# Kernel optimization log

Hardware: AMD Instinct MI355X
Metric: run time of the kernel (lower is better)

## Reference

```python
import jax, jax.numpy as jnp
import numpy as np

LAMBDA = 1.0          # lambda_param
SIGMA = 1.0           # RBF bandwidth (sigkernel convention: exp(-||x-y||^2 / sigma))
DYADIC_ORDER = 2
F = 2 ** DYADIC_ORDER # dyadic refinement factor per time axis

B, M_POP, DIM, SEQ_LEN = 4, 16, 8, 65


def _rbf_gram(X, Y):
    # X: (m, L, d), Y: (n, L, d) -> static kernel Gram (m, n, L, L)
    sx = jnp.sum(X * X, -1)                       # (m, L)
    sy = jnp.sum(Y * Y, -1)                       # (n, L)
    inner = jnp.einsum('isd,jtd->ijst', X, Y)     # (m, n, L, L)
    d2 = sx[:, None, :, None] + sy[None, :, None, :] - 2.0 * inner
    return jnp.exp(-d2 / SIGMA)


def _increments(G):
    # double increment of the static Gram over time, then dyadic refinement
    inc = G[..., 1:, 1:] + G[..., :-1, :-1] - G[..., 1:, :-1] - G[..., :-1, 1:]
    inc = jnp.repeat(jnp.repeat(inc, F, axis=-2), F, axis=-1) / (F * F)
    return inc  # (..., S, S) with S = F*(L-1)


def _solve_pde(M):
    # Goursat PDE explicit finite-difference scheme (as in sigkernel):
    # K[i+1,j+1] = (K[i+1,j]+K[i,j+1])*(1 + m/2 + m^2/12) - K[i,j]*(1 - m^2/12)
    dtype = M.dtype
    S = M.shape[0]

    def row_step(prev_row, m_row):
        def cell(k_left, inp):
            k00, k01, m = inp
            a = 1.0 + 0.5 * m + m * m * (1.0 / 12.0)
            b = 1.0 - m * m * (1.0 / 12.0)
            k_new = (k_left + k01) * a - k00 * b
            return k_new, k_new
        _, tail = jax.lax.scan(cell, jnp.asarray(1.0, dtype),
                               (prev_row[:-1], prev_row[1:], m_row))
        new_row = jnp.concatenate([jnp.ones((1,), dtype), tail])
        return new_row, None

    row0 = jnp.ones((S + 1,), dtype)
    last_row, _ = jax.lax.scan(row_step, row0, M)
    return last_row[-1]


def _gram_sig(X, Y):
    # signature kernel Gram matrix: X (m,L,d), Y (n,L,d) -> (m,n)
    Minc = _increments(_rbf_gram(X, Y))
    return jax.vmap(jax.vmap(_solve_pde))(Minc)


def setup_inputs() -> dict:
    key = jax.random.key(0)
    k1, k2 = jax.random.split(key)
    generated_samples = jax.random.normal(k1, (B, M_POP, DIM, SEQ_LEN), dtype=jnp.float32)
    real_sample = jax.random.normal(k2, (B, DIM, SEQ_LEN), dtype=jnp.float32)
    return {"generated_samples": generated_samples, "real_sample": real_sample}


def reference(generated_samples, real_sample):
    # generated_samples: (B, m, dim, L); real_sample: (B, dim, L)
    gen = jnp.swapaxes(generated_samples, -1, -2)          # (B, m, L, d)
    real = jnp.swapaxes(real_sample, -1, -2)[:, None]      # (B, 1, L, d)
    m = gen.shape[1]
    K_XX = jax.vmap(_gram_sig)(gen, gen)                   # (B, m, m)
    K_XY = jax.vmap(_gram_sig)(gen, real)                  # (B, m, 1)
    self_sim = (jnp.sum(K_XX, axis=(-1, -2))
                - jnp.trace(K_XX, axis1=-2, axis2=-1)) / (m * (m - 1))
    cross_sim = jnp.mean(K_XY, axis=(-1, -2))
    return jnp.mean(LAMBDA / 2.0 * self_sim - cross_sim)
```

## Files before the change

### kernel.cpp

```cpp
#include <hip/hip_runtime.h>


#define SEQ   65
#define DIMS  8
#define MPOP  16
#define NBATCH 4
#define NPAIR_XX 120
#define NBLOCKS (NBATCH*(NPAIR_XX + MPOP))
#define MST 67

__device__ __forceinline__ float wave_shr1(float x) {
    int xi = __builtin_bit_cast(int, x);
    int r  = __builtin_amdgcn_update_dpp(xi, xi, 0x138 , 0xF, 0xF, false);
    return __builtin_bit_cast(float, r);
}

__device__ __forceinline__ int clamp63(int v) {
    return v < 0 ? 0 : (v > 63 ? 63 : v);
}

__global__ __launch_bounds__(256) void sigker_kernel(
    const float* __restrict__ gen,
    const float* __restrict__ realp,
    float* __restrict__ out)
{
    __shared__ float YsL[SEQ][DIMS];
    __shared__ float MmL[64 * MST];

    const int tid = threadIdx.x;
    const int I   = tid & 63;
    const int c   = tid >> 6;
    const int bid = blockIdx.x;

    int b, ii, jj; bool cross;
    if (bid < NBATCH * NPAIR_XX) {
        b = bid / NPAIR_XX;
        int p = bid % NPAIR_XX;
        int i = 0, acc = 0;
        while (p >= acc + (MPOP - 1 - i)) { acc += (MPOP - 1 - i); ++i; }
        ii = i; jj = i + 1 + (p - acc); cross = false;
    } else {
        int t = bid - NBATCH * NPAIR_XX;
        b = t / MPOP; ii = t % MPOP; jj = 0; cross = true;
    }

    const float* Xg = gen + (size_t)(b * MPOP + ii) * (DIMS * SEQ);
    const float* Yg = cross ? (realp + (size_t)b * (DIMS * SEQ))
                            : (gen + (size_t)(b * MPOP + jj) * (DIMS * SEQ));

    for (int f = tid; f < SEQ * DIMS; f += 256) {
        int d = f / SEQ, s = f - d * SEQ;
        YsL[s][d] = Yg[f];
    }
    float x0[DIMS], x1[DIMS];
    #pragma unroll
    for (int d = 0; d < DIMS; ++d) {
        x0[d] = Xg[d * SEQ + I];
        x1[d] = Xg[d * SEQ + I + 1];
    }
    __syncthreads();

    {
        float* mrow = &MmL[I * MST];
        const int t0 = c * 16;
        float e0p, e1p;
        {
            float d0 = 0.f, d1 = 0.f;
            #pragma unroll
            for (int d = 0; d < DIMS; ++d) {
                float y = YsL[t0][d];
                float a0 = x0[d] - y; d0 += a0 * a0;
                float a1 = x1[d] - y; d1 += a1 * a1;
            }
            e0p = __expf(-d0); e1p = __expf(-d1);
        }
        #pragma unroll
        for (int t = 1; t <= 16; ++t) {
            float d0 = 0.f, d1 = 0.f;
            #pragma unroll
            for (int d = 0; d < DIMS; ++d) {
                float y = YsL[t0 + t][d];
                float a0 = x0[d] - y; d0 += a0 * a0;
                float a1 = x1[d] - y; d1 += a1 * a1;
            }
            float e0 = __expf(-d0), e1 = __expf(-d1);
            mrow[t0 + t - 1] = (e1 + e0p - e1p - e0) * (1.0f / 16.0f);
            e0p = e0; e1p = e1;
        }
    }
    __syncthreads();
    if (tid >= 64) return;

    const float* mrow = &MmL[I * MST];
    float l0 = 1.f, l1 = 1.f, l2 = 1.f, l3 = 1.f;
    float b0 = 1.f, b1 = 1.f, b2 = 1.f, b3 = 1.f;
    float cnext = 1.f;

#define STEP(DTv, MV) do {                                              \
        float t0_ = wave_shr1(b0);                                      \
        float t1_ = wave_shr1(b1);                                      \
        float t2_ = wave_shr1(b2);                                      \
        float t3_ = wave_shr1(b3);                                      \
        float cc_ = cnext; cnext = t3_;                                 \
        if (I == 0) { t0_ = t1_ = t2_ = t3_ = 1.f; cc_ = 1.f; }         \
        int J_ = (DTv) - I;                                             \
        if ((unsigned)J_ < 64u) {                                       \
            if (J_ == 0) cc_ = 1.f;                                     \
            float m_   = (MV);                                          \
            float q12_ = m_ * m_ * (1.0f / 12.0f);                      \
            float a_   = 1.0f + 0.5f * m_ + q12_;                       \
            float nb_  = q12_ - 1.0f;                                   \
            float u0_ = a_ * t0_ + nb_ * cc_;                           \
            float u1_ = a_ * t1_ + nb_ * t0_;                           \
            float u2_ = a_ * t2_ + nb_ * t1_;                           \
            float u3_ = a_ * t3_ + nb_ * t2_;                           \
            float q1_ = a_ * l0 + u0_;                                  \
            float q2_ = a_ * q1_ + u1_;                                 \
            float q3_ = a_ * q2_ + u2_;                                 \
            float q4_ = a_ * q3_ + u3_;                                 \
            u0_ = a_ * q1_ + nb_ * l0;  u1_ = a_ * q2_ + nb_ * q1_;     \
            u2_ = a_ * q3_ + nb_ * q2_; u3_ = a_ * q4_ + nb_ * q3_;     \
            float r1_ = a_ * l1 + u0_;                                  \
            float r2_ = a_ * r1_ + u1_;                                 \
            float r3_ = a_ * r2_ + u2_;                                 \
            float r4_ = a_ * r3_ + u3_;                                 \
            u0_ = a_ * r1_ + nb_ * l1;  u1_ = a_ * r2_ + nb_ * r1_;     \
            u2_ = a_ * r3_ + nb_ * r2_; u3_ = a_ * r4_ + nb_ * r3_;     \
            float s1_ = a_ * l2 + u0_;                                  \
            float s2_ = a_ * s1_ + u1_;                                 \
            float s3_ = a_ * s2_ + u2_;                                 \
            float s4_ = a_ * s3_ + u3_;                                 \
            u0_ = a_ * s1_ + nb_ * l2;  u1_ = a_ * s2_ + nb_ * s1_;     \
            u2_ = a_ * s3_ + nb_ * s2_; u3_ = a_ * s4_ + nb_ * s3_;     \
            float v1_ = a_ * l3 + u0_;                                  \
            float v2_ = a_ * v1_ + u1_;                                 \
            float v3_ = a_ * v2_ + u2_;                                 \
            float v4_ = a_ * v3_ + u3_;                                 \
            b0 = v1_; b1 = v2_; b2 = v3_; b3 = v4_;                     \
            l0 = q4_; l1 = r4_; l2 = s4_; l3 = v4_;                     \
        }                                                               \
    } while (0)

    float m0 = mrow[clamp63(0 - I)];
    float m1 = mrow[clamp63(1 - I)];
    float m2 = mrow[clamp63(2 - I)];
    float m3 = mrow[clamp63(3 - I)];

    for (int g = 0; g < 32; ++g) {
        const int DT0 = g * 4;
        float n0 = mrow[clamp63(DT0 + 4 - I)];
        float n1 = mrow[clamp63(DT0 + 5 - I)];
        float n2 = mrow[clamp63(DT0 + 6 - I)];
        float n3 = mrow[clamp63(DT0 + 7 - I)];
        STEP(DT0 + 0, m0);
        STEP(DT0 + 1, m1);
        STEP(DT0 + 2, m2);
        STEP(DT0 + 3, m3);
        m0 = n0; m1 = n1; m2 = n2; m3 = n3;
    }
#undef STEP

    if (tid == 63) {
        float w = cross ? (-1.0f / 32.0f) : (1.0f / 480.0f);
        atomicAdd(out, w * b3);
    }
}

extern "C" void kernel_launch(void* const* d_in, const int* in_sizes, int n_in,
                              void* d_out, int out_size, void* d_ws, size_t ws_size,
                              hipStream_t stream) {
    const float* gen   = (const float*)d_in[0];
    const float* realp = (const float*)d_in[1];
    if (n_in >= 2 && in_sizes[0] == NBATCH * DIMS * SEQ) {
        gen   = (const float*)d_in[1];
        realp = (const float*)d_in[0];
    }
    float* out = (float*)d_out;
    hipMemsetAsync(out, 0, sizeof(float), stream);
    sigker_kernel<<<NBLOCKS, 256, 0, stream>>>(gen, realp, out);
}
```

Before: 96.28 us.

## Use single-wave blocks and replace atomic accumulation with a workspace reduction

Each block shrinks from 256 threads to one 64-lane wave. That wave computes the whole increment row per lane, which removes the block barrier and the idle waves during the PDE sweep. The atomicAdd and the memset are replaced by per-block writes to a workspace, summed by a second small reduction kernel. In exchange, each block does four times more serial Gram work per lane and the launch gains an extra kernel.

```diff
diff --git a/kernel.cpp b/kernel.cpp
--- a/kernel.cpp
+++ b/kernel.cpp
@@ -19,17 +19,16 @@
     return v < 0 ? 0 : (v > 63 ? 63 : v);
 }
 
-__global__ __launch_bounds__(256) void sigker_kernel(
+__global__ __launch_bounds__(64, 1) void sigker_kernel(
     const float* __restrict__ gen,
     const float* __restrict__ realp,
-    float* __restrict__ out)
+    float* __restrict__ ws)
 {
     __shared__ float YsL[SEQ][DIMS];
     __shared__ float MmL[64 * MST];
 
     const int tid = threadIdx.x;
-    const int I   = tid & 63;
-    const int c   = tid >> 6;
+    const int I   = tid;
     const int bid = blockIdx.x;
 
     int b, ii, jj; bool cross;
@@ -48,7 +47,7 @@
     const float* Yg = cross ? (realp + (size_t)b * (DIMS * SEQ))
                             : (gen + (size_t)(b * MPOP + jj) * (DIMS * SEQ));
 
-    for (int f = tid; f < SEQ * DIMS; f += 256) {
+    for (int f = tid; f < SEQ * DIMS; f += 64) {
         int d = f / SEQ, s = f - d * SEQ;
         YsL[s][d] = Yg[f];
     }
@@ -60,38 +59,32 @@
     }
     __syncthreads();
 
+    float* mrow = &MmL[I * MST];
+    float e0p, e1p;
     {
-        float* mrow = &MmL[I * MST];
-        const int t0 = c * 16;
-        float e0p, e1p;
-        {
-            float d0 = 0.f, d1 = 0.f;
-            #pragma unroll
-            for (int d = 0; d < DIMS; ++d) {
-                float y = YsL[t0][d];
-                float a0 = x0[d] - y; d0 += a0 * a0;
-                float a1 = x1[d] - y; d1 += a1 * a1;
-            }
-            e0p = __expf(-d0); e1p = __expf(-d1);
+        float d0 = 0.f, d1 = 0.f;
+        #pragma unroll
+        for (int d = 0; d < DIMS; ++d) {
+            float y = YsL[0][d];
+            float a0 = x0[d] - y; d0 += a0 * a0;
+            float a1 = x1[d] - y; d1 += a1 * a1;
         }
+        e0p = __expf(-d0); e1p = __expf(-d1);
+    }
+    #pragma unroll 8
+    for (int t = 1; t < SEQ; ++t) {
+        float d0 = 0.f, d1 = 0.f;
         #pragma unroll
-        for (int t = 1; t <= 16; ++t) {
-            float d0 = 0.f, d1 = 0.f;
-            #pragma unroll
-            for (int d = 0; d < DIMS; ++d) {
-                float y = YsL[t0 + t][d];
-                float a0 = x0[d] - y; d0 += a0 * a0;
-                float a1 = x1[d] - y; d1 += a1 * a1;
-            }
-            float e0 = __expf(-d0), e1 = __expf(-d1);
-            mrow[t0 + t - 1] = (e1 + e0p - e1p - e0) * (1.0f / 16.0f);
-            e0p = e0; e1p = e1;
+        for (int d = 0; d < DIMS; ++d) {
+            float y = YsL[t][d];
+            float a0 = x0[d] - y; d0 += a0 * a0;
+            float a1 = x1[d] - y; d1 += a1 * a1;
         }
+        float e0 = __expf(-d0), e1 = __expf(-d1);
+        mrow[t - 1] = (e1 + e0p - e1p - e0) * (1.0f / 16.0f);
+        e0p = e0; e1p = e1;
     }
-    __syncthreads();
-    if (tid >= 64) return;
 
-    const float* mrow = &MmL[I * MST];
     float l0 = 1.f, l1 = 1.f, l2 = 1.f, l3 = 1.f;
     float b0 = 1.f, b1 = 1.f, b2 = 1.f, b3 = 1.f;
     float cnext = 1.f;
@@ -162,8 +155,19 @@
 
     if (tid == 63) {
         float w = cross ? (-1.0f / 32.0f) : (1.0f / 480.0f);
-        atomicAdd(out, w * b3);
+        ws[bid] = w * b3;
     }
+}
+
+__global__ __launch_bounds__(64, 1) void sigker_reduce(
+    const float* __restrict__ ws, float* __restrict__ out)
+{
+    const int lane = threadIdx.x;
+    float s = 0.f;
+    for (int k = lane; k < NBLOCKS; k += 64) s += ws[k];
+    #pragma unroll
+    for (int off = 32; off >= 1; off >>= 1) s += __shfl_xor(s, off);
+    if (lane == 0) out[0] = s;
 }
 
 extern "C" void kernel_launch(void* const* d_in, const int* in_sizes, int n_in,
@@ -175,7 +179,8 @@
         gen   = (const float*)d_in[1];
         realp = (const float*)d_in[0];
     }
+    float* ws  = (float*)d_ws;
     float* out = (float*)d_out;
-    hipMemsetAsync(out, 0, sizeof(float), stream);
-    sigker_kernel<<<NBLOCKS, 256, 0, stream>>>(gen, realp, out);
+    sigker_kernel<<<NBLOCKS, 64, 0, stream>>>(gen, realp, ws);
+    sigker_reduce<<<1, 64, 0, stream>>>(ws, out);
 }
```

After: 91.08 us. 1.06x faster.
